# Optimization experiments

Hardware: AMD Instinct MI355X
Metric: run time of the kernel (lower is better)

Reference implementation:

```python
import jax, jax.numpy as jnp
import numpy as np

B, S, D_MODEL, H = 4, 1024, 1024, 16
DEPTH = D_MODEL // H


def head_scales():
    # np.arange(0.1, 10 + 0.01, 9.9 / (H - 1)) -> exactly H values from 0.1 to 10.0
    return jnp.asarray(np.arange(0.1, 10 + 0.01, 9.9 / (H - 1)), dtype=jnp.float32)


def setup_inputs() -> dict:
    key = jax.random.key(0)
    ks = jax.random.split(key, 14)
    sd = 1.0 / np.sqrt(D_MODEL)
    inp = {
        "v": jax.random.normal(ks[0], (B, S, D_MODEL), jnp.float32),
        "k": jax.random.normal(ks[1], (B, S, D_MODEL), jnp.float32),
        "q": jax.random.normal(ks[2], (B, S, D_MODEL), jnp.float32),
        # pairwise distance-like weights in [0, 1)
        "weight": jax.random.uniform(ks[3], (B, S, S), jnp.float32),
        # binary padding mask, broadcastable to (B, H, S, S); 1 = masked
        "mask": (jax.random.uniform(ks[4], (B, 1, 1, S)) < 0.1).astype(jnp.float32),
        "Wq": jax.random.normal(ks[5], (D_MODEL, D_MODEL), jnp.float32) * sd,
        "bq": jnp.zeros((D_MODEL,), jnp.float32),
        "Wk": jax.random.normal(ks[6], (D_MODEL, D_MODEL), jnp.float32) * sd,
        "bk": jnp.zeros((D_MODEL,), jnp.float32),
        "Wv": jax.random.normal(ks[7], (D_MODEL, D_MODEL), jnp.float32) * sd,
        "bv": jnp.zeros((D_MODEL,), jnp.float32),
        "Wo": jax.random.normal(ks[8], (D_MODEL, D_MODEL), jnp.float32) * sd,
        "bo": jnp.zeros((D_MODEL,), jnp.float32),
    }
    return inp


def reference(v, k, q, weight, mask, Wq, bq, Wk, bk, Wv, bv, Wo, bo):
    def split_heads(x):  # (B, S, D) -> (B, H, S, depth)
        return x.reshape(B, -1, H, DEPTH).transpose(0, 2, 1, 3)

    qh = split_heads(q @ Wq + bq)
    kh = split_heads(k @ Wk + bk)
    vh = split_heads(v @ Wv + bv)

    # shift_distance[b,h,i,j] = weight[b,i,j] * scale[h]
    scales = head_scales()  # (H,)
    bias = weight[:, None, :, :] * scales[None, :, None, None]  # (B, H, S, S)

    logits = jnp.einsum("bhqd,bhkd->bhqk", qh, kh) / jnp.sqrt(
        jnp.asarray(DEPTH, jnp.float32)
    )
    logits = logits + bias + mask * (-1e9)
    attn = jax.nn.softmax(logits, axis=-1)  # (B, H, S, S)
    out = jnp.einsum("bhqk,bhkd->bhqd", attn, vh)  # (B, H, S, depth)
    out = out.transpose(0, 2, 1, 3).reshape(B, -1, D_MODEL)
    return out @ Wo + bo
```

## Files before the change

### kernel.cpp

```cpp
#include <hip/hip_runtime.h>
#include <hip/hip_fp16.h>

#define DEV __device__ __forceinline__

typedef _Float16 f16x8 __attribute__((ext_vector_type(8)));
typedef _Float16 f16x4 __attribute__((ext_vector_type(4)));
typedef float f32x4 __attribute__((ext_vector_type(4)));

DEV void gload16(void* lds, const void* g) {
  __builtin_amdgcn_global_load_lds((__attribute__((address_space(1))) const void*)g,
                                   (__attribute__((address_space(3))) void*)lds,
                                   16, 0, 0);
}

DEV f32x4 mfma16(f16x8 a, f16x8 b, f32x4 c) {
  return __builtin_amdgcn_mfma_f32_16x16x32_f16(a, b, c, 0, 0, 0);
}

__global__ __launch_bounds__(256) void transw_kernel(
    const float* __restrict__ W0, const float* __restrict__ W1,
    const float* __restrict__ W2, const float* __restrict__ W3,
    _Float16* __restrict__ Wt) {
  __shared__ float tile[32][33];
  const float* W = (blockIdx.z == 0) ? W0 : (blockIdx.z == 1) ? W1
                 : (blockIdx.z == 2) ? W2 : W3;
  _Float16* dst = Wt + (size_t)blockIdx.z * (1024 * 1024);
  const int tx = threadIdx.x & 31, ty = threadIdx.x >> 5;
  const int n0 = blockIdx.x * 32, k0 = blockIdx.y * 32;
#pragma unroll
  for (int i = 0; i < 4; ++i)
    tile[ty + i * 8][tx] = W[(size_t)(k0 + ty + i * 8) * 1024 + n0 + tx];
  __syncthreads();
#pragma unroll
  for (int i = 0; i < 4; ++i)
    dst[(size_t)(n0 + ty + i * 8) * 1024 + k0 + tx] = (_Float16)tile[tx][ty + i * 8];
}

__global__ __launch_bounds__(256) void wcast_kernel(const float* __restrict__ W,
                                                    _Float16* __restrict__ Wh) {
  const size_t i = (size_t)(blockIdx.x * 256 + threadIdx.x) * 8;
  float4 a = *(const float4*)(W + i);
  float4 b = *(const float4*)(W + i + 4);
  f16x8 o;
  o[0] = (_Float16)a.x; o[1] = (_Float16)a.y; o[2] = (_Float16)a.z; o[3] = (_Float16)a.w;
  o[4] = (_Float16)b.x; o[5] = (_Float16)b.y; o[6] = (_Float16)b.z; o[7] = (_Float16)b.w;
  *(f16x8*)(Wh + i) = o;
}

template <bool AF32>
DEV void gemm_core(const void* __restrict__ Aptr, const _Float16* __restrict__ Bt,
                   _Float16* Al, _Float16* Bl, int m0, int n0, f32x4 (&acc)[4][4]) {
  constexpr int AS = AF32 ? 40 : 32;
  const int t = threadIdx.x;
  const int l = t & 63, w = t >> 6;
  const int wr = w >> 1, wc = w & 1;
  const int lo = l & 15, lg = l >> 4;

  for (int ks = 0; ks < 1024; ks += 32) {
    __syncthreads();
    gload16(&Bl[t * 8], Bt + (size_t)(n0 + (t >> 2)) * 1024 + ks + (t & 3) * 8);
    gload16(&Bl[(t + 256) * 8], Bt + (size_t)(n0 + (t >> 2) + 64) * 1024 + ks + (t & 3) * 8);
    if constexpr (AF32) {
      const float* Ag = (const float*)Aptr;
      const int row = t >> 1, c0 = (t & 1) * 16;
      const float4* src = (const float4*)(Ag + (size_t)(m0 + row) * 1024 + ks + c0);
      float4 f0 = src[0], f1 = src[1], f2 = src[2], f3 = src[3];
      f16x8 v0, v1;
      v0[0] = (_Float16)f0.x; v0[1] = (_Float16)f0.y; v0[2] = (_Float16)f0.z; v0[3] = (_Float16)f0.w;
      v0[4] = (_Float16)f1.x; v0[5] = (_Float16)f1.y; v0[6] = (_Float16)f1.z; v0[7] = (_Float16)f1.w;
      v1[0] = (_Float16)f2.x; v1[1] = (_Float16)f2.y; v1[2] = (_Float16)f2.z; v1[3] = (_Float16)f2.w;
      v1[4] = (_Float16)f3.x; v1[5] = (_Float16)f3.y; v1[6] = (_Float16)f3.z; v1[7] = (_Float16)f3.w;
      *(f16x8*)&Al[row * AS + c0] = v0;
      *(f16x8*)&Al[row * AS + c0 + 8] = v1;
    } else {
      const _Float16* Ag = (const _Float16*)Aptr;
      gload16(&Al[t * 8], Ag + (size_t)(m0 + (t >> 2)) * 1024 + ks + (t & 3) * 8);
      gload16(&Al[(t + 256) * 8], Ag + (size_t)(m0 + (t >> 2) + 64) * 1024 + ks + (t & 3) * 8);
    }
    __syncthreads();

    f16x8 af[4], bf[4];
#pragma unroll
    for (int mi = 0; mi < 4; ++mi)
      af[mi] = *(const f16x8*)&Al[(wr * 64 + mi * 16 + lo) * AS + lg * 8];
#pragma unroll
    for (int ni = 0; ni < 4; ++ni)
      bf[ni] = *(const f16x8*)&Bl[(wc * 64 + ni * 16 + lo) * 32 + lg * 8];
#pragma unroll
    for (int mi = 0; mi < 4; ++mi)
#pragma unroll
      for (int ni = 0; ni < 4; ++ni)
        acc[mi][ni] = mfma16(af[mi], bf[ni], acc[mi][ni]);
  }
}

__global__ __launch_bounds__(256) void proj_kernel(
    const float* __restrict__ qin, const float* __restrict__ kin,
    const float* __restrict__ vin, const _Float16* __restrict__ Wt,
    const float* __restrict__ bq, const float* __restrict__ bk,
    const float* __restrict__ bv, _Float16* __restrict__ Qh,
    _Float16* __restrict__ Kt, _Float16* __restrict__ Vt) {
  __shared__ __attribute__((aligned(16))) _Float16 Al[128 * 40];
  __shared__ __attribute__((aligned(16))) _Float16 Bl[128 * 32];
  const int lin = blockIdx.x + (blockIdx.y << 3) + (blockIdx.z << 8);
  const int work = (lin & 7) * 96 + (lin >> 3);
  const int z = work >> 8;
  const int m0 = ((work & 255) >> 3) * 128;
  const int n0 = (work & 7) * 128;

  const float* A = (z == 0) ? qin : (z == 1) ? kin : vin;
  const _Float16* Bt = Wt + (size_t)z * (1 << 20);
  const float* bias = (z == 0) ? bq : (z == 1) ? bk : bv;
  _Float16* C = (z == 0) ? Qh : (z == 1) ? Kt : Vt;

  f32x4 acc[4][4];
#pragma unroll
  for (int i = 0; i < 4; ++i)
#pragma unroll
    for (int j = 0; j < 4; ++j) acc[i][j] = (f32x4){0.f, 0.f, 0.f, 0.f};
  gemm_core<true>(A, Bt, Al, Bl, m0, n0, acc);

  const int l = threadIdx.x & 63, w = threadIdx.x >> 6;
  const int wr = w >> 1, wc = w & 1;
  const int lo = l & 15, lg = l >> 4;
#pragma unroll
  for (int mi = 0; mi < 4; ++mi) {
#pragma unroll
    for (int ni = 0; ni < 4; ++ni) {
      const int col = n0 + wc * 64 + ni * 16 + lo;
      const int rowb = m0 + wr * 64 + mi * 16 + lg * 4;
      const float bc = bias[col];
      const int h = col >> 6, d = col & 63;
#pragma unroll
      for (int r = 0; r < 4; ++r) {
        const float vv = acc[mi][ni][r] + bc;
        const int m = rowb + r;
        const int b = m >> 10, s = m & 1023;
        const size_t slab = (size_t)(b * 16 + h) * 65536;
        if (z == 0) {
          C[slab + (size_t)s * 64 + d] = (_Float16)vv;
        } else if (z == 1) {
          C[slab + (size_t)(s >> 6) * 4096 + (size_t)(s & 63) * 64 +
            (((d >> 3) ^ (s & 7)) << 3) + (d & 7)] = (_Float16)vv;
        } else {
          C[slab + (size_t)(s >> 6) * 4096 + (size_t)d * 64 +
            ((((s >> 3) & 7) ^ (d & 7)) << 3) + (s & 7)] = (_Float16)vv;
        }
      }
    }
  }
}

__global__ __launch_bounds__(256) void outproj_kernel(
    const _Float16* __restrict__ AO, const _Float16* __restrict__ Bt,
    const float* __restrict__ bias, float* __restrict__ out) {
  __shared__ __attribute__((aligned(16))) _Float16 Al[128 * 32];
  __shared__ __attribute__((aligned(16))) _Float16 Bl[128 * 32];
  const int lin = blockIdx.x + (blockIdx.y << 3);
  const int work = (lin & 7) * 32 + (lin >> 3);
  const int m0 = (work >> 3) * 128;
  const int n0 = (work & 7) * 128;
  f32x4 acc[4][4];
#pragma unroll
  for (int i = 0; i < 4; ++i)
#pragma unroll
    for (int j = 0; j < 4; ++j) acc[i][j] = (f32x4){0.f, 0.f, 0.f, 0.f};
  gemm_core<false>(AO, Bt, Al, Bl, m0, n0, acc);

  const int l = threadIdx.x & 63, w = threadIdx.x >> 6;
  const int wr = w >> 1, wc = w & 1;
  const int lo = l & 15, lg = l >> 4;
#pragma unroll
  for (int mi = 0; mi < 4; ++mi) {
#pragma unroll
    for (int ni = 0; ni < 4; ++ni) {
      const int col = n0 + wc * 64 + ni * 16 + lo;
      const int rowb = m0 + wr * 64 + mi * 16 + lg * 4;
      const float bc = bias[col];
#pragma unroll
      for (int r = 0; r < 4; ++r)
        out[(size_t)(rowb + r) * 1024 + col] = acc[mi][ni][r] + bc;
    }
  }
}

template <int NSPLIT>
__global__ __launch_bounds__(512, 4) void attn_kernel(
    const _Float16* __restrict__ Qh, const _Float16* __restrict__ Kt,
    const _Float16* __restrict__ Vt, const _Float16* __restrict__ Wh,
    const float* __restrict__ mask, void* __restrict__ Oout,
    float2* __restrict__ Sst) {
  __shared__ __attribute__((aligned(16))) _Float16 Kl[2][4096];
  __shared__ __attribute__((aligned(16))) _Float16 Vl[2][4096];
  __shared__ __attribute__((aligned(16))) _Float16 Pl[8][16][72];
  const int t = threadIdx.x, l = t & 63, w = t >> 6;
  const int lo = l & 15, lg = l >> 4;
  const int bh = blockIdx.y, b = bh >> 4, h = bh & 15;
  const int q0w = blockIdx.x * 128 + w * 16;
  const int sp = (NSPLIT > 1) ? blockIdx.z : 0;
  constexpr int NKT = 16 / NSPLIT;
  const int kt0 = sp * NKT;
  constexpr float L2E = 1.44269504089f;
  const float scale = 0.1f + (float)h * (9.9f / 15.0f);
  const float cS = 0.125f * L2E;
  const float cW = scale * L2E;
  const float cM = -1e9f * L2E;
  const _Float16* Kslab = Kt + (size_t)bh * 65536;
  const _Float16* Vslab = Vt + (size_t)bh * 65536;
  const _Float16* Wb = Wh + ((size_t)b << 20);
  const float* Mb = mask + (size_t)b * 1024;
  const int qrow = q0w + lg * 4;
  const int sl = lg ^ (lo & 7);

  const f16x8 qf0 = *(const f16x8*)(Qh + (size_t)bh * 65536 + (q0w + lo) * 64 + lg * 8);
  const f16x8 qf1 = *(const f16x8*)(Qh + (size_t)bh * 65536 + (q0w + lo) * 64 + 32 + lg * 8);

  f32x4 oacc[4];
#pragma unroll
  for (int di = 0; di < 4; ++di) oacc[di] = (f32x4){0.f, 0.f, 0.f, 0.f};
  float mrun[4], lsum[4];
#pragma unroll
  for (int r = 0; r < 4; ++r) { mrun[r] = -1e38f; lsum[r] = 0.f; }

  gload16(&Kl[0][t * 8], Kslab + (size_t)kt0 * 4096 + t * 8);
  gload16(&Vl[0][t * 8], Vslab + (size_t)kt0 * 4096 + t * 8);
  __syncthreads();

  for (int it = 0; it < NKT; ++it) {
    const int kt = kt0 + it;
    const int cur = it & 1;
    if (it + 1 < NKT) {
      gload16(&Kl[cur ^ 1][t * 8], Kslab + (size_t)(kt + 1) * 4096 + t * 8);
      gload16(&Vl[cur ^ 1][t * 8], Vslab + (size_t)(kt + 1) * 4096 + t * 8);
    }
    const int kv0 = kt * 64;
    const _Float16* Kb = Kl[cur];
    const _Float16* Vb = Vl[cur];

    float sv[4][4];
    float tm[4] = {-1e38f, -1e38f, -1e38f, -1e38f};
#pragma unroll
    for (int ni = 0; ni < 4; ++ni) {
      const int key = kv0 + ni * 16 + lo;
      const float mkv = Mb[key] * cM;
      float wgt[4];
#pragma unroll
      for (int r = 0; r < 4; ++r)
        wgt[r] = (float)Wb[(size_t)(qrow + r) * 1024 + key];
      const int kr = ni * 16 + lo;
      f16x8 kf0 = *(const f16x8*)(Kb + kr * 64 + sl * 8);
      f16x8 kf1 = *(const f16x8*)(Kb + kr * 64 + (sl ^ 4) * 8);
      f32x4 s = (f32x4){0.f, 0.f, 0.f, 0.f};
      s = mfma16(qf0, kf0, s);
      s = mfma16(qf1, kf1, s);
#pragma unroll
      for (int r = 0; r < 4; ++r) {
        const float x = s[r] * cS + wgt[r] * cW + mkv;
        sv[ni][r] = x;
        tm[r] = fmaxf(tm[r], x);
      }
    }
#pragma unroll
    for (int st = 1; st < 16; st <<= 1)
#pragma unroll
      for (int r = 0; r < 4; ++r) tm[r] = fmaxf(tm[r], __shfl_xor(tm[r], st));
    float delta = tm[0] - mrun[0];
#pragma unroll
    for (int r = 1; r < 4; ++r) delta = fmaxf(delta, tm[r] - mrun[r]);
    if (!__all(delta <= 8.0f)) {
      float fr[4];
#pragma unroll
      for (int r = 0; r < 4; ++r) {
        const float mn = fmaxf(mrun[r], tm[r]);
        fr[r] = exp2f(mrun[r] - mn);
        mrun[r] = mn;
        lsum[r] *= fr[r];
      }
#pragma unroll
      for (int di = 0; di < 4; ++di)
#pragma unroll
        for (int r = 0; r < 4; ++r) oacc[di][r] *= fr[r];
    }
#pragma unroll
    for (int ni = 0; ni < 4; ++ni)
#pragma unroll
      for (int r = 0; r < 4; ++r) {
        const float p = exp2f(sv[ni][r] - mrun[r]);
        lsum[r] += p;
        Pl[w][lg * 4 + r][ni * 16 + lo] = (_Float16)p;
      }
    const f16x8 pa0 = *(const f16x8*)(&Pl[w][lo][lg * 8]);
    const f16x8 pa1 = *(const f16x8*)(&Pl[w][lo][32 + lg * 8]);
    __builtin_amdgcn_s_setprio(1);
#pragma unroll
    for (int di = 0; di < 4; ++di) {
      const int d = di * 16 + lo;
      f16x8 vf0 = *(const f16x8*)(Vb + d * 64 + sl * 8);
      f16x8 vf1 = *(const f16x8*)(Vb + d * 64 + (sl ^ 4) * 8);
      oacc[di] = mfma16(pa0, vf0, oacc[di]);
      oacc[di] = mfma16(pa1, vf1, oacc[di]);
    }
    __builtin_amdgcn_s_setprio(0);
    __syncthreads();
  }

#pragma unroll
  for (int st = 1; st < 16; st <<= 1)
#pragma unroll
    for (int r = 0; r < 4; ++r) lsum[r] += __shfl_xor(lsum[r], st);

  if constexpr (NSPLIT > 1) {
    if (lo == 0) {
#pragma unroll
      for (int r = 0; r < 4; ++r)
        Sst[(size_t)sp * 65536 + bh * 1024 + qrow + r] = make_float2(mrun[r], lsum[r]);
    }
    _Float16* Op = (_Float16*)Oout + (size_t)sp * (64ull * 1024 * 64);
#pragma unroll
    for (int r = 0; r < 4; ++r) {
      const float inv = 1.0f / lsum[r];
#pragma unroll
      for (int di = 0; di < 4; ++di)
        Op[((size_t)bh * 1024 + qrow + r) * 64 + di * 16 + lo] =
            (_Float16)(oacc[di][r] * inv);
    }
  } else {
    _Float16* AO = (_Float16*)Oout;
#pragma unroll
    for (int r = 0; r < 4; ++r) {
      const float inv = 1.0f / lsum[r];
#pragma unroll
      for (int di = 0; di < 4; ++di)
        AO[((size_t)(b * 1024) + qrow + r) * 1024 + h * 64 + di * 16 + lo] =
            (_Float16)(oacc[di][r] * inv);
    }
  }
}

__global__ __launch_bounds__(256) void merge_kernel(
    const _Float16* __restrict__ Op, const float2* __restrict__ Sst,
    _Float16* __restrict__ AO) {
  const int idx = blockIdx.x * 256 + threadIdx.x;
  const int dc = idx & 15;
  const int qq = (idx >> 4) & 1023;
  const int bh = idx >> 14;
  const int b = bh >> 4, h = bh & 15;
  const float2 s1 = Sst[bh * 1024 + qq];
  const float2 s2 = Sst[65536 + bh * 1024 + qq];
  const float m = fmaxf(s1.x, s2.x);
  float w1 = exp2f(s1.x - m) * s1.y;
  float w2 = exp2f(s2.x - m) * s2.y;
  const float inv = 1.f / (w1 + w2);
  w1 *= inv; w2 *= inv;
  const size_t o = ((size_t)bh * 1024 + qq) * 64 + dc * 4;
  const f16x4 o1 = *(const f16x4*)(Op + o);
  const f16x4 o2 = *(const f16x4*)(Op + (64ull * 1024 * 64) + o);
  f16x4 r;
#pragma unroll
  for (int j = 0; j < 4; ++j)
    r[j] = (_Float16)(w1 * (float)o1[j] + w2 * (float)o2[j]);
  *(f16x4*)(AO + ((size_t)(b * 1024 + qq) * 1024 + h * 64 + dc * 4)) = r;
}

extern "C" void kernel_launch(void* const* d_in, const int* in_sizes, int n_in,
                              void* d_out, int out_size, void* d_ws, size_t ws_size,
                              hipStream_t stream) {
  (void)in_sizes; (void)n_in; (void)out_size;
  const float* v      = (const float*)d_in[0];
  const float* k      = (const float*)d_in[1];
  const float* q      = (const float*)d_in[2];
  const float* weight = (const float*)d_in[3];
  const float* mask   = (const float*)d_in[4];
  const float* Wq = (const float*)d_in[5];
  const float* bq = (const float*)d_in[6];
  const float* Wk = (const float*)d_in[7];
  const float* bk = (const float*)d_in[8];
  const float* Wv = (const float*)d_in[9];
  const float* bv = (const float*)d_in[10];
  const float* Wo = (const float*)d_in[11];
  const float* bo = (const float*)d_in[12];
  float* out = (float*)d_out;

  const size_t MB = 1ull << 20;
  char* ws = (char*)d_ws;
  _Float16* Wt = (_Float16*)ws;
  _Float16* Qh = (_Float16*)(ws + 8 * MB);
  _Float16* Kt = (_Float16*)(ws + 16 * MB);
  _Float16* Vt = (_Float16*)(ws + 24 * MB);
  _Float16* Wh = (_Float16*)(ws + 32 * MB);

  transw_kernel<<<dim3(32, 32, 4), 256, 0, stream>>>(Wq, Wk, Wv, Wo, Wt);
  wcast_kernel<<<2048, 256, 0, stream>>>(weight, Wh);
  proj_kernel<<<dim3(8, 32, 3), 256, 0, stream>>>(q, k, v, Wt, bq, bk, bv, Qh, Kt, Vt);

  if (ws_size >= 57 * MB) {
    _Float16* Op  = (_Float16*)(ws + 40 * MB);
    float2*   Sst = (float2*)(ws + 56 * MB);
    _Float16* AO  = Qh;
    attn_kernel<2><<<dim3(8, 64, 2), 512, 0, stream>>>(Qh, Kt, Vt, Wh, mask, Op, Sst);
    merge_kernel<<<4096, 256, 0, stream>>>(Op, Sst, AO);
    outproj_kernel<<<dim3(8, 32), 256, 0, stream>>>(AO, Wt + 3 * (1 << 20), bo, out);
  } else {
    _Float16* AO = (_Float16*)(ws + 40 * MB);
    attn_kernel<1><<<dim3(8, 64, 1), 512, 0, stream>>>(Qh, Kt, Vt, Wh, mask, AO, nullptr);
    outproj_kernel<<<dim3(8, 32), 256, 0, stream>>>(AO, Wt + 3 * (1 << 20), bo, out);
  }
}
```

Measured before the change: 154.4 us.

## Pre-cast QKV inputs to fp16 and use 64-row tiles in output projection

Measured after the change: 152.6 us. No clear change (-1.2%).

```diff
diff --git a/kernel.cpp b/kernel.cpp
--- a/kernel.cpp
+++ b/kernel.cpp
@@ -15,6 +15,13 @@
 
 DEV f32x4 mfma16(f16x8 a, f16x8 b, f32x4 c) {
   return __builtin_amdgcn_mfma_f32_16x16x32_f16(a, b, c, 0, 0, 0);
+}
+
+DEV f16x8 cvt8(float4 a, float4 b) {
+  f16x8 o;
+  o[0] = (_Float16)a.x; o[1] = (_Float16)a.y; o[2] = (_Float16)a.z; o[3] = (_Float16)a.w;
+  o[4] = (_Float16)b.x; o[5] = (_Float16)b.y; o[6] = (_Float16)b.z; o[7] = (_Float16)b.w;
+  return o;
 }
 
 __global__ __launch_bounds__(256) void transw_kernel(
@@ -41,19 +48,29 @@
   const size_t i = (size_t)(blockIdx.x * 256 + threadIdx.x) * 8;
   float4 a = *(const float4*)(W + i);
   float4 b = *(const float4*)(W + i + 4);
-  f16x8 o;
-  o[0] = (_Float16)a.x; o[1] = (_Float16)a.y; o[2] = (_Float16)a.z; o[3] = (_Float16)a.w;
-  o[4] = (_Float16)b.x; o[5] = (_Float16)b.y; o[6] = (_Float16)b.z; o[7] = (_Float16)b.w;
-  *(f16x8*)(Wh + i) = o;
-}
-
-template <bool AF32>
+  *(f16x8*)(Wh + i) = cvt8(a, b);
+}
+
+__global__ __launch_bounds__(256) void qkvcast_kernel(
+    const float* __restrict__ q, const float* __restrict__ k,
+    const float* __restrict__ v, _Float16* __restrict__ Ah) {
+  const float* src = (blockIdx.y == 0) ? q : (blockIdx.y == 1) ? k : v;
+  _Float16* dst = Ah + (size_t)blockIdx.y * (4096ull * 1024);
+  const size_t i = (size_t)(blockIdx.x * 256 + threadIdx.x) * 8;
+  float4 a = *(const float4*)(src + i);
+  float4 b = *(const float4*)(src + i + 4);
+  *(f16x8*)(dst + i) = cvt8(a, b);
+}
+
+template <int BM, bool AF32>
 DEV void gemm_core(const void* __restrict__ Aptr, const _Float16* __restrict__ Bt,
-                   _Float16* Al, _Float16* Bl, int m0, int n0, f32x4 (&acc)[4][4]) {
+                   _Float16* Al, _Float16* Bl, int m0, int n0,
+                   f32x4 (&acc)[4][4]) {
   constexpr int AS = AF32 ? 40 : 32;
+  constexpr int WR = BM / 64, WC = 4 / WR, NI = (128 / WC) / 16;
   const int t = threadIdx.x;
   const int l = t & 63, w = t >> 6;
-  const int wr = w >> 1, wc = w & 1;
+  const int wr = w / WC, wc = w % WC;
   const int lo = l & 15, lg = l >> 4;
 
   for (int ks = 0; ks < 1024; ks += 32) {
@@ -65,41 +82,39 @@
       const int row = t >> 1, c0 = (t & 1) * 16;
       const float4* src = (const float4*)(Ag + (size_t)(m0 + row) * 1024 + ks + c0);
       float4 f0 = src[0], f1 = src[1], f2 = src[2], f3 = src[3];
-      f16x8 v0, v1;
-      v0[0] = (_Float16)f0.x; v0[1] = (_Float16)f0.y; v0[2] = (_Float16)f0.z; v0[3] = (_Float16)f0.w;
-      v0[4] = (_Float16)f1.x; v0[5] = (_Float16)f1.y; v0[6] = (_Float16)f1.z; v0[7] = (_Float16)f1.w;
-      v1[0] = (_Float16)f2.x; v1[1] = (_Float16)f2.y; v1[2] = (_Float16)f2.z; v1[3] = (_Float16)f2.w;
-      v1[4] = (_Float16)f3.x; v1[5] = (_Float16)f3.y; v1[6] = (_Float16)f3.z; v1[7] = (_Float16)f3.w;
-      *(f16x8*)&Al[row * AS + c0] = v0;
-      *(f16x8*)&Al[row * AS + c0 + 8] = v1;
+      *(f16x8*)&Al[row * AS + c0] = cvt8(f0, f1);
+      *(f16x8*)&Al[row * AS + c0 + 8] = cvt8(f2, f3);
     } else {
       const _Float16* Ag = (const _Float16*)Aptr;
       gload16(&Al[t * 8], Ag + (size_t)(m0 + (t >> 2)) * 1024 + ks + (t & 3) * 8);
-      gload16(&Al[(t + 256) * 8], Ag + (size_t)(m0 + (t >> 2) + 64) * 1024 + ks + (t & 3) * 8);
+      if constexpr (BM == 128)
+        gload16(&Al[(t + 256) * 8], Ag + (size_t)(m0 + (t >> 2) + 64) * 1024 + ks + (t & 3) * 8);
     }
     __syncthreads();
 
-    f16x8 af[4], bf[4];
+    f16x8 af[4], bf[NI];
 #pragma unroll
     for (int mi = 0; mi < 4; ++mi)
       af[mi] = *(const f16x8*)&Al[(wr * 64 + mi * 16 + lo) * AS + lg * 8];
 #pragma unroll
-    for (int ni = 0; ni < 4; ++ni)
-      bf[ni] = *(const f16x8*)&Bl[(wc * 64 + ni * 16 + lo) * 32 + lg * 8];
+    for (int ni = 0; ni < NI; ++ni)
+      bf[ni] = *(const f16x8*)&Bl[(wc * (NI * 16) + ni * 16 + lo) * 32 + lg * 8];
 #pragma unroll
     for (int mi = 0; mi < 4; ++mi)
 #pragma unroll
-      for (int ni = 0; ni < 4; ++ni)
+      for (int ni = 0; ni < NI; ++ni)
         acc[mi][ni] = mfma16(af[mi], bf[ni], acc[mi][ni]);
   }
 }
 
+template <bool AHALF>
 __global__ __launch_bounds__(256) void proj_kernel(
-    const float* __restrict__ qin, const float* __restrict__ kin,
-    const float* __restrict__ vin, const _Float16* __restrict__ Wt,
-    const float* __restrict__ bq, const float* __restrict__ bk,
-    const float* __restrict__ bv, _Float16* __restrict__ Qh,
-    _Float16* __restrict__ Kt, _Float16* __restrict__ Vt) {
+    const _Float16* __restrict__ Ah, const float* __restrict__ qin,
+    const float* __restrict__ kin, const float* __restrict__ vin,
+    const _Float16* __restrict__ Wt, const float* __restrict__ bq,
+    const float* __restrict__ bk, const float* __restrict__ bv,
+    _Float16* __restrict__ Qh, _Float16* __restrict__ Kt,
+    _Float16* __restrict__ Vt) {
   __shared__ __attribute__((aligned(16))) _Float16 Al[128 * 40];
   __shared__ __attribute__((aligned(16))) _Float16 Bl[128 * 32];
   const int lin = blockIdx.x + (blockIdx.y << 3) + (blockIdx.z << 8);
@@ -108,7 +123,6 @@
   const int m0 = ((work & 255) >> 3) * 128;
   const int n0 = (work & 7) * 128;
 
-  const float* A = (z == 0) ? qin : (z == 1) ? kin : vin;
   const _Float16* Bt = Wt + (size_t)z * (1 << 20);
   const float* bias = (z == 0) ? bq : (z == 1) ? bk : bv;
   _Float16* C = (z == 0) ? Qh : (z == 1) ? Kt : Vt;
@@ -118,7 +132,12 @@
   for (int i = 0; i < 4; ++i)
 #pragma unroll
     for (int j = 0; j < 4; ++j) acc[i][j] = (f32x4){0.f, 0.f, 0.f, 0.f};
-  gemm_core<true>(A, Bt, Al, Bl, m0, n0, acc);
+  if constexpr (AHALF) {
+    gemm_core<128, false>(Ah + (size_t)z * (4096ull * 1024), Bt, Al, Bl, m0, n0, acc);
+  } else {
+    const float* A = (z == 0) ? qin : (z == 1) ? kin : vin;
+    gemm_core<128, true>(A, Bt, Al, Bl, m0, n0, acc);
+  }
 
   const int l = threadIdx.x & 63, w = threadIdx.x >> 6;
   const int wr = w >> 1, wc = w & 1;
@@ -154,28 +173,28 @@
 __global__ __launch_bounds__(256) void outproj_kernel(
     const _Float16* __restrict__ AO, const _Float16* __restrict__ Bt,
     const float* __restrict__ bias, float* __restrict__ out) {
-  __shared__ __attribute__((aligned(16))) _Float16 Al[128 * 32];
+  __shared__ __attribute__((aligned(16))) _Float16 Al[64 * 32];
   __shared__ __attribute__((aligned(16))) _Float16 Bl[128 * 32];
   const int lin = blockIdx.x + (blockIdx.y << 3);
-  const int work = (lin & 7) * 32 + (lin >> 3);
-  const int m0 = (work >> 3) * 128;
+  const int work = (lin & 7) * 64 + (lin >> 3);
+  const int m0 = (work >> 3) * 64;
   const int n0 = (work & 7) * 128;
   f32x4 acc[4][4];
 #pragma unroll
   for (int i = 0; i < 4; ++i)
 #pragma unroll
     for (int j = 0; j < 4; ++j) acc[i][j] = (f32x4){0.f, 0.f, 0.f, 0.f};
-  gemm_core<false>(AO, Bt, Al, Bl, m0, n0, acc);
+  gemm_core<64, false>(AO, Bt, Al, Bl, m0, n0, acc);
 
   const int l = threadIdx.x & 63, w = threadIdx.x >> 6;
-  const int wr = w >> 1, wc = w & 1;
+  const int wc = w;
   const int lo = l & 15, lg = l >> 4;
 #pragma unroll
   for (int mi = 0; mi < 4; ++mi) {
 #pragma unroll
-    for (int ni = 0; ni < 4; ++ni) {
-      const int col = n0 + wc * 64 + ni * 16 + lo;
-      const int rowb = m0 + wr * 64 + mi * 16 + lg * 4;
+    for (int ni = 0; ni < 2; ++ni) {
+      const int col = n0 + wc * 32 + ni * 16 + lo;
+      const int rowb = m0 + mi * 16 + lg * 4;
       const float bc = bias[col];
 #pragma unroll
       for (int r = 0; r < 4; ++r)
@@ -388,21 +407,26 @@
   _Float16* Kt = (_Float16*)(ws + 16 * MB);
   _Float16* Vt = (_Float16*)(ws + 24 * MB);
   _Float16* Wh = (_Float16*)(ws + 32 * MB);
+  _Float16* Ah = (_Float16*)(ws + 40 * MB);
+  _Float16* Op = (_Float16*)(ws + 40 * MB);
+  float2*  Sst = (float2*)(ws + 56 * MB);
+  _Float16* AO = Qh;
 
   transw_kernel<<<dim3(32, 32, 4), 256, 0, stream>>>(Wq, Wk, Wv, Wo, Wt);
   wcast_kernel<<<2048, 256, 0, stream>>>(weight, Wh);
-  proj_kernel<<<dim3(8, 32, 3), 256, 0, stream>>>(q, k, v, Wt, bq, bk, bv, Qh, Kt, Vt);
-
-  if (ws_size >= 57 * MB) {
-    _Float16* Op  = (_Float16*)(ws + 40 * MB);
-    float2*   Sst = (float2*)(ws + 56 * MB);
-    _Float16* AO  = Qh;
+
+  if (ws_size >= 64 * MB) {
+    qkvcast_kernel<<<dim3(2048, 3), 256, 0, stream>>>(q, k, v, Ah);
+    proj_kernel<true><<<dim3(8, 32, 3), 256, 0, stream>>>(Ah, q, k, v, Wt, bq, bk, bv,
+                                                          Qh, Kt, Vt);
     attn_kernel<2><<<dim3(8, 64, 2), 512, 0, stream>>>(Qh, Kt, Vt, Wh, mask, Op, Sst);
     merge_kernel<<<4096, 256, 0, stream>>>(Op, Sst, AO);
-    outproj_kernel<<<dim3(8, 32), 256, 0, stream>>>(AO, Wt + 3 * (1 << 20), bo, out);
+    outproj_kernel<<<dim3(8, 64), 256, 0, stream>>>(AO, Wt + 3 * (1 << 20), bo, out);
   } else {
-    _Float16* AO = (_Float16*)(ws + 40 * MB);
-    attn_kernel<1><<<dim3(8, 64, 1), 512, 0, stream>>>(Qh, Kt, Vt, Wh, mask, AO, nullptr);
-    outproj_kernel<<<dim3(8, 32), 256, 0, stream>>>(AO, Wt + 3 * (1 << 20), bo, out);
-  }
-}
+    _Float16* AO2 = (_Float16*)(ws + 40 * MB);
+    proj_kernel<false><<<dim3(8, 32, 3), 256, 0, stream>>>(nullptr, q, k, v, Wt, bq, bk,
+                                                           bv, Qh, Kt, Vt);
+    attn_kernel<1><<<dim3(8, 64, 1), 512, 0, stream>>>(Qh, Kt, Vt, Wh, mask, AO2, nullptr);
+    outproj_kernel<<<dim3(8, 64), 256, 0, stream>>>(AO2, Wt + 3 * (1 << 20), bo, out);
+  }
+}
```
